# Kernel tuning notes

Measured on AMD Instinct MI355X. Metric: run time of the kernel, lower is better.

Reference implementation:

```python
import jax, jax.numpy as jnp
import numpy as np

DIM = 1024
NUM_HEADS = 16
HEAD_DIM = DIM // NUM_HEADS
BATCH = 4
SEQ = 2048
EPS = 1e-6


def rotate_half(x):
    # interleaved-pair rotation: (..., d) -> view (..., d//2, 2), swap with sign
    x = x.reshape(*x.shape[:-1], -1, 2)
    x1, x2 = jnp.split(x, 2, axis=-1)  # each (..., d//2, 1)
    x = jnp.concatenate([-x2, x1], axis=-1)
    return x.reshape(*x.shape[:-2], -1)


def apply_rope(x, cos, sin):
    # x: [B,S,H,D], cos/sin: [S,D]
    cos = cos[None, :, None, :].astype(x.dtype)
    sin = sin[None, :, None, :].astype(x.dtype)
    return x * cos + rotate_half(x) * sin


def rms_norm(x, w):
    var = jnp.mean(jnp.square(x), axis=-1, keepdims=True)
    return x * jax.lax.rsqrt(var + EPS) * w


def setup_inputs() -> dict:
    key = jax.random.key(0)
    ks = jax.random.split(key, 8)
    s = 0.02
    return {
        "x": jax.random.normal(ks[0], (BATCH, SEQ, DIM), jnp.float32),
        "rope_cos": jnp.cos(jnp.arange(SEQ, dtype=jnp.float32)[:, None] *
                            (1.0 / (10000.0 ** (jnp.repeat(jnp.arange(HEAD_DIM // 2, dtype=jnp.float32), 2) * 2 / HEAD_DIM)))[None, :]),
        "rope_sin": jnp.sin(jnp.arange(SEQ, dtype=jnp.float32)[:, None] *
                            (1.0 / (10000.0 ** (jnp.repeat(jnp.arange(HEAD_DIM // 2, dtype=jnp.float32), 2) * 2 / HEAD_DIM)))[None, :]),
        "qkv_w": jax.random.normal(ks[1], (3 * DIM, DIM), jnp.float32) * s,
        "qkv_b": jax.random.normal(ks[2], (3 * DIM,), jnp.float32) * s,
        "proj_w": jax.random.normal(ks[3], (DIM, DIM), jnp.float32) * s,
        "proj_b": jax.random.normal(ks[4], (DIM,), jnp.float32) * s,
        "q_norm_w": jnp.ones((HEAD_DIM,), jnp.float32),
        "k_norm_w": jnp.ones((HEAD_DIM,), jnp.float32),
    }


def reference(x, rope_cos, rope_sin, qkv_w, qkv_b, proj_w, proj_b, q_norm_w, k_norm_w):
    B, S, C = x.shape
    H, D = NUM_HEADS, HEAD_DIM
    qkv = x @ qkv_w.T + qkv_b                      # [B,S,3C]
    qkv = qkv.reshape(B, S, 3, H, D)
    q, k, v = qkv[:, :, 0], qkv[:, :, 1], qkv[:, :, 2]  # [B,S,H,D]
    q = apply_rope(rms_norm(q, q_norm_w), rope_cos, rope_sin)
    k = apply_rope(rms_norm(k, k_norm_w), rope_cos, rope_sin)
    scale = 1.0 / np.sqrt(D).astype(np.float32)
    attn = jnp.einsum('bqhd,bkhd->bhqk', q.astype(jnp.float32), k.astype(jnp.float32))
    attn = jax.nn.softmax(attn * scale, axis=-1).astype(x.dtype)
    out = jnp.einsum('bhqk,bkhd->bqhd', attn, v).reshape(B, S, C)
    return out @ proj_w.T + proj_b
```

## Files before the change

### kernel.cpp

```cpp
#include <hip/hip_runtime.h>
#include <math.h>
#include <type_traits>

#define DIM 1024
#define NH 16
#define HD 64
#define BATCH 4
#define SEQ 2048
#define EPS 1e-6f

typedef __attribute__((ext_vector_type(8))) short short8;
typedef __attribute__((ext_vector_type(4))) short short4v;
typedef __attribute__((ext_vector_type(4))) float float4v;

__device__ inline unsigned short f2bf(float f) {
    unsigned u = __float_as_uint(f);
    u += 0x7FFF + ((u >> 16) & 1);
    return (unsigned short)(u >> 16);
}
__device__ inline float bf2f(unsigned short b) {
    return __uint_as_float(((unsigned)b) << 16);
}
__device__ inline unsigned pk2bf(float lo, float hi) {
    unsigned ul = __float_as_uint(lo) + 0x8000u;
    unsigned uh = __float_as_uint(hi) + 0x8000u;
    return __builtin_amdgcn_perm(uh, ul, 0x07060302u);
}

#if __has_builtin(__builtin_amdgcn_exp2f)
#define EXP2F(x) __builtin_amdgcn_exp2f(x)
#else
#define EXP2F(x) exp2f(x)
#endif

#if __has_builtin(__builtin_amdgcn_mfma_f32_16x16x16bf16_1k)
__device__ inline float4v mfma16(short4v a, short4v b, float4v c) {
    return __builtin_amdgcn_mfma_f32_16x16x16bf16_1k(a, b, c, 0, 0, 0);
}
#elif __has_builtin(__builtin_amdgcn_mfma_f32_16x16x16_bf16)
__device__ inline float4v mfma16(short4v a, short4v b, float4v c) {
    return __builtin_amdgcn_mfma_f32_16x16x16_bf16(a, b, c, 0, 0, 0);
}
#else
__device__ inline float4v mfma16(short4v a, short4v b, float4v c) {
    asm volatile("v_mfma_f32_16x16x16_bf16 %0, %1, %2, %0\n\ts_nop 4"
                 : "+v"(c) : "v"(a), "v"(b));
    return c;
}
#endif

#define GLDS16(gp, lp) __builtin_amdgcn_global_load_lds( \
    (const __attribute__((address_space(1))) void*)(gp), \
    (__attribute__((address_space(3))) void*)(lp), 16, 0, 0)

__global__ __launch_bounds__(256) void prep_all(
    const float* __restrict__ x, const float* __restrict__ qkv_w,
    const float* __restrict__ proj_w,
    const float* __restrict__ cos_t, const float* __restrict__ sin_t,
    unsigned short* __restrict__ xb, unsigned short* __restrict__ qkvwb,
    unsigned short* __restrict__ projwb, unsigned* __restrict__ csP)
{
    const int bid = blockIdx.x;
    if (bid < 8192) {
        int i = bid * 256 + threadIdx.x;
        float4 f = ((const float4*)x)[i];
        ushort4 o;
        o.x = f2bf(f.x); o.y = f2bf(f.y); o.z = f2bf(f.z); o.w = f2bf(f.w);
        ((ushort4*)xb)[i] = o;
    } else if (bid < 8192 + 3072) {
        const int rn = bid - 8192;
        int ro = rn;
        if (rn < 2048) {
            const int head = rn >> 6, c = rn & 63, j = c >> 4, cl = c & 15;
            ro = (head << 6) + ((j & 1) + 2 * cl + 32 * (j >> 1));
        }
        float4 f = ((const float4*)(qkv_w + (long)ro * DIM))[threadIdx.x];
        ushort4 o;
        o.x = f2bf(f.x); o.y = f2bf(f.y); o.z = f2bf(f.z); o.w = f2bf(f.w);
        ((ushort4*)(qkvwb + (long)rn * DIM))[threadIdx.x] = o;
    } else if (bid < 8192 + 3072 + 1024) {
        int i = (bid - 11264) * 256 + threadIdx.x;
        float4 f = ((const float4*)proj_w)[i];
        ushort4 o;
        o.x = f2bf(f.x); o.y = f2bf(f.y); o.z = f2bf(f.z); o.w = f2bf(f.w);
        ((ushort4*)projwb)[i] = o;
    } else {
        int i = (bid - 12288) * 256 + threadIdx.x;
        int a = i >> 11, s = i & 2047;
        float c = cos_t[s * 64 + 2 * a], sn = sin_t[s * 64 + 2 * a];
        csP[a * SEQ + s] = ((unsigned)f2bf(sn) << 16) | f2bf(c);
    }
}

__global__ __launch_bounds__(256) void gemm_qkv_fused(
    const unsigned short* __restrict__ A, const unsigned short* __restrict__ W,
    const float* __restrict__ bias, const unsigned* __restrict__ csP,
    const float* __restrict__ qw, const float* __restrict__ kw,
    unsigned short* __restrict__ q, unsigned short* __restrict__ k,
    unsigned short* __restrict__ vt)
{
    __shared__ __align__(16) unsigned short As[128 * 32];
    __shared__ __align__(16) unsigned short Bs[128 * 32];

    const int t    = threadIdx.x;
    const int lane = t & 63;
    const int w    = t >> 6;
    const int row0 = blockIdx.y * 128;
    const int col0 = blockIdx.x * 128;
    const int wr   = (w & 1) * 64;
    const int wc   = (w >> 1) * 64;
    const int cl   = lane & 15;
    const int quad = lane >> 4;

    float4v acc[4][4];
#pragma unroll
    for (int i = 0; i < 4; ++i)
#pragma unroll
        for (int j = 0; j < 4; ++j) acc[i][j] = (float4v){0.f, 0.f, 0.f, 0.f};

    const int off1 = t * 16, off2 = 4096 + t * 16;
    const int r1 = off1 >> 6, c1 = off1 & 63;
    const int r2 = off2 >> 6, c2 = off2 & 63;
    const char* Ab = (const char*)A + (long)row0 * DIM * 2;
    const char* Wb = (const char*)W + (long)col0 * DIM * 2;
    const long  ks = DIM * 2;

    for (int k0 = 0; k0 < DIM; k0 += 32) {
        const long kb = (long)k0 * 2;
        GLDS16(Ab + (long)r1 * ks + kb + c1, (char*)As + off1);
        GLDS16(Ab + (long)r2 * ks + kb + c2, (char*)As + off2);
        GLDS16(Wb + (long)r1 * ks + kb + c1, (char*)Bs + off1);
        GLDS16(Wb + (long)r2 * ks + kb + c2, (char*)Bs + off2);
        __syncthreads();

        short8 af[4], bfr[4];
#pragma unroll
        for (int i = 0; i < 4; ++i)
            af[i] = *(const short8*)&As[(wr + i * 16 + cl) * 32 + quad * 8];
#pragma unroll
        for (int j = 0; j < 4; ++j)
            bfr[j] = *(const short8*)&Bs[(wc + j * 16 + cl) * 32 + quad * 8];
#pragma unroll
        for (int i = 0; i < 4; ++i)
#pragma unroll
            for (int j = 0; j < 4; ++j)
                acc[i][j] = __builtin_amdgcn_mfma_f32_16x16x32_bf16(af[i], bfr[j], acc[i][j], 0, 0, 0);
        __syncthreads();
    }

    const int gcol  = col0 + wc;
    const int b     = row0 >> 11;
    const int srow0 = (row0 & 2047) + wr;

    if (gcol < 2 * DIM) {
        const bool isq = (gcol < DIM);
        const int  h   = (isq ? gcol : gcol - DIM) >> 6;
        const float* nw = isq ? qw : kw;
        const float scale = isq ? 0.180336880f : 1.0f;
        unsigned short* dst = (isq ? q : k) + (long)(b * NH + h) * SEQ * 64;

        float bjv[4];
#pragma unroll
        for (int j = 0; j < 4; ++j)
            bjv[j] = bias[gcol + (j & 1) + 2 * cl + 32 * (j >> 1)];
#pragma unroll
        for (int i = 0; i < 4; ++i)
#pragma unroll
            for (int j = 0; j < 4; ++j)
#pragma unroll
                for (int r = 0; r < 4; ++r) acc[i][j][r] += bjv[j];

        float rinv[4][4];
#pragma unroll
        for (int i = 0; i < 4; ++i)
#pragma unroll
            for (int r = 0; r < 4; ++r) {
                float ss = acc[i][0][r] * acc[i][0][r];
                ss = fmaf(acc[i][1][r], acc[i][1][r], ss);
                ss = fmaf(acc[i][2][r], acc[i][2][r], ss);
                ss = fmaf(acc[i][3][r], acc[i][3][r], ss);
                ss += __shfl_xor(ss, 1, 64);
                ss += __shfl_xor(ss, 2, 64);
                ss += __shfl_xor(ss, 4, 64);
                ss += __shfl_xor(ss, 8, 64);
                rinv[i][r] = rsqrtf(ss * (1.f / 64.f) + EPS) * scale;
            }

        const float nwe[2] = { nw[2 * cl],     nw[32 + 2 * cl] };
        const float nwo[2] = { nw[2 * cl + 1], nw[33 + 2 * cl] };

#pragma unroll
        for (int i = 0; i < 4; ++i) {
            const int sb = srow0 + i * 16 + quad * 4;
#pragma unroll
            for (int jp = 0; jp < 2; ++jp) {
                uint4 cs4 = *(const uint4*)(csP + (long)(jp * 16 + cl) * SEQ + sb);
#pragma unroll
                for (int r = 0; r < 4; ++r) {
                    float g  = rinv[i][r];
                    float xe = acc[i][2 * jp][r]     * g * nwe[jp];
                    float xo = acc[i][2 * jp + 1][r] * g * nwo[jp];
                    unsigned u = (r == 0) ? cs4.x : (r == 1) ? cs4.y : (r == 2) ? cs4.z : cs4.w;
                    float c  = bf2f((unsigned short)(u & 0xffff));
                    float sn = bf2f((unsigned short)(u >> 16));
                    float oe = fmaf(xe, c, -(xo * sn));
                    float oo = fmaf(xo, c,   xe * sn);
                    *(unsigned*)(dst + (long)(sb + r) * 64 + jp * 32 + 2 * cl) = pk2bf(oe, oo);
                }
            }
        }
    } else {
        const int h = (gcol - 2 * DIM) >> 6;
        float bjv[4];
#pragma unroll
        for (int j = 0; j < 4; ++j) bjv[j] = bias[gcol + j * 16 + cl];
        unsigned short* vdst = vt + (long)(b * NH + h) * SEQ * 64
                                  + (long)(srow0 >> 6) * 4096;
#pragma unroll
        for (int j = 0; j < 4; ++j)
#pragma unroll
            for (int ip = 0; ip < 2; ++ip) {
                const int i0 = 2 * ip;
                uint4 st;
                st.x = pk2bf(acc[i0][j][0] + bjv[j],     acc[i0][j][1] + bjv[j]);
                st.y = pk2bf(acc[i0][j][2] + bjv[j],     acc[i0][j][3] + bjv[j]);
                st.z = pk2bf(acc[i0 + 1][j][0] + bjv[j], acc[i0 + 1][j][1] + bjv[j]);
                st.w = pk2bf(acc[i0 + 1][j][2] + bjv[j], acc[i0 + 1][j][3] + bjv[j]);
                *(uint4*)(vdst + (j * 2 + ip) * 512 + lane * 8) = st;
            }
    }
}

__global__ __launch_bounds__(256) void gemm_proj(
    const unsigned short* __restrict__ A, const unsigned short* __restrict__ W,
    const float* __restrict__ bias, float* __restrict__ C)
{
    __shared__ __align__(16) unsigned short As[128 * 32];
    __shared__ __align__(16) unsigned short Bs[128 * 32];

    const int t    = threadIdx.x;
    const int lane = t & 63;
    const int w    = t >> 6;
    const int row0 = blockIdx.y * 128;
    const int col0 = blockIdx.x * 128;
    const int wr   = (w & 1) * 64;
    const int wc   = (w >> 1) * 64;

    float4v acc[4][4];
#pragma unroll
    for (int i = 0; i < 4; ++i)
#pragma unroll
        for (int j = 0; j < 4; ++j) acc[i][j] = (float4v){0.f, 0.f, 0.f, 0.f};

    const int off1 = t * 16, off2 = 4096 + t * 16;
    const int r1 = off1 >> 6, c1 = off1 & 63;
    const int r2 = off2 >> 6, c2 = off2 & 63;
    const char* Ab = (const char*)A + (long)row0 * DIM * 2;
    const char* Wb = (const char*)W + (long)col0 * DIM * 2;
    const long  ks = DIM * 2;

    for (int k0 = 0; k0 < DIM; k0 += 32) {
        const long kb = (long)k0 * 2;
        GLDS16(Ab + (long)r1 * ks + kb + c1, (char*)As + off1);
        GLDS16(Ab + (long)r2 * ks + kb + c2, (char*)As + off2);
        GLDS16(Wb + (long)r1 * ks + kb + c1, (char*)Bs + off1);
        GLDS16(Wb + (long)r2 * ks + kb + c2, (char*)Bs + off2);
        __syncthreads();

        short8 af[4], bfr[4];
#pragma unroll
        for (int i = 0; i < 4; ++i)
            af[i] = *(const short8*)&As[(wr + i * 16 + (lane & 15)) * 32 + (lane >> 4) * 8];
#pragma unroll
        for (int j = 0; j < 4; ++j)
            bfr[j] = *(const short8*)&Bs[(wc + j * 16 + (lane & 15)) * 32 + (lane >> 4) * 8];
#pragma unroll
        for (int i = 0; i < 4; ++i)
#pragma unroll
            for (int j = 0; j < 4; ++j)
                acc[i][j] = __builtin_amdgcn_mfma_f32_16x16x32_bf16(af[i], bfr[j], acc[i][j], 0, 0, 0);
        __syncthreads();
    }

    const int qd = lane >> 4, cl = lane & 15;
#pragma unroll
    for (int j = 0; j < 4; ++j) {
        const int col = col0 + wc + j * 16 + cl;
        const float bj = bias[col];
#pragma unroll
        for (int i = 0; i < 4; ++i) {
            const long rr = row0 + wr + i * 16 + qd * 4;
#pragma unroll
            for (int r = 0; r < 4; ++r)
                C[(rr + r) * (long)DIM + col] = acc[i][j][r] + bj;
        }
    }
}

__global__ __launch_bounds__(256) void flash_mfma(
    const unsigned short* __restrict__ q, const unsigned short* __restrict__ k,
    const unsigned short* __restrict__ vt, unsigned short* __restrict__ out)
{
    __shared__ __align__(16) unsigned short Qs[2][128 * 32];
    __shared__ __align__(16) unsigned short Ks[2][64 * 32];
    __shared__ __align__(16) unsigned short Vts[64 * 64];

    const int t    = threadIdx.x;
    const int lane = t & 63;
    const int w    = t >> 6;
    const int bh   = blockIdx.y;
    const int b    = bh >> 4;
    const int h    = bh & 15;
    const int q0   = blockIdx.x * 128;
    const int cl   = lane & 15;
    const int quad = lane >> 4;

    const char* qb  = (const char*)(q  + (long)bh * SEQ * 64);
    const char* kb  = (const char*)(k  + (long)bh * SEQ * 64);
    const char* vtb = (const char*)(vt + (long)bh * SEQ * 64);

#pragma unroll
    for (int rd = 0; rd < 2; ++rd) {
        const int off = rd * 4096 + t * 16;
        const int row = off >> 6, cb = off & 63;
#pragma unroll
        for (int hf = 0; hf < 2; ++hf)
            GLDS16(qb + (long)(q0 + row) * 128 + hf * 64 + cb, (char*)Qs[hf] + off);
    }
    __syncthreads();

    short8 aq[2][2];
#pragma unroll
    for (int qg = 0; qg < 2; ++qg)
#pragma unroll
        for (int hf = 0; hf < 2; ++hf)
            aq[qg][hf] = *(const short8*)&Qs[hf][(w * 32 + qg * 16 + cl) * 32 + quad * 8];

    const short4v ones = (short4v){(short)0x3F80, (short)0x3F80, (short)0x3F80, (short)0x3F80};

    float4v o[2][4], o4[2];
#pragma unroll
    for (int qg = 0; qg < 2; ++qg) {
        o4[qg] = (float4v){0.f, 0.f, 0.f, 0.f};
#pragma unroll
        for (int i = 0; i < 4; ++i) o[qg][i] = (float4v){0.f, 0.f, 0.f, 0.f};
    }

    const int soff = t * 16, srow = soff >> 6, scb = soff & 63;

    for (int kt = 0; kt < SEQ / 64; ++kt) {
#pragma unroll
        for (int hf = 0; hf < 2; ++hf)
            GLDS16(kb + (long)(kt * 64 + srow) * 128 + hf * 64 + scb, (char*)Ks[hf] + soff);
        GLDS16(vtb + (long)kt * 8192 + t * 16,        (char*)Vts + t * 16);
        GLDS16(vtb + (long)kt * 8192 + 4096 + t * 16, (char*)Vts + 4096 + t * 16);
        __syncthreads();

        short4v pa[2][4];
#pragma unroll
        for (int j = 0; j < 4; ++j) {
            short8 a0 = *(const short8*)&Ks[0][(j * 16 + cl) * 32 + quad * 8];
            short8 a1 = *(const short8*)&Ks[1][(j * 16 + cl) * 32 + quad * 8];
#pragma unroll
            for (int qg = 0; qg < 2; ++qg) {
                float4v z = (float4v){0.f, 0.f, 0.f, 0.f};
                z = __builtin_amdgcn_mfma_f32_16x16x32_bf16(a0, aq[qg][0], z, 0, 0, 0);
                float4v s = __builtin_amdgcn_mfma_f32_16x16x32_bf16(a1, aq[qg][1], z, 0, 0, 0);
                float p0 = EXP2F(s[0]), p1 = EXP2F(s[1]);
                float p2 = EXP2F(s[2]), p3 = EXP2F(s[3]);
                unsigned lo = pk2bf(p0, p1), hi = pk2bf(p2, p3);
                pa[qg][j] = __builtin_bit_cast(short4v, ((unsigned long long)hi << 32) | lo);
                o4[qg] = mfma16(ones, pa[qg][j], o4[qg]);
            }
        }

#pragma unroll
        for (int fi = 0; fi < 4; ++fi) {
#pragma unroll
            for (int fjp = 0; fjp < 2; ++fjp) {
                short8 vv = *(const short8*)&Vts[(fi * 2 + fjp) * 512 + lane * 8];
                short4v va = __builtin_shufflevector(vv, vv, 0, 1, 2, 3);
                short4v vb = __builtin_shufflevector(vv, vv, 4, 5, 6, 7);
#pragma unroll
                for (int qg = 0; qg < 2; ++qg) {
                    o[qg][fi] = mfma16(va, pa[qg][2 * fjp],     o[qg][fi]);
                    o[qg][fi] = mfma16(vb, pa[qg][2 * fjp + 1], o[qg][fi]);
                }
            }
        }
        __syncthreads();
    }

#pragma unroll
    for (int qg = 0; qg < 2; ++qg) {
        const float inv = 1.f / o4[qg][0];
        unsigned short* orow = out + ((long)b * SEQ + q0 + w * 32 + qg * 16 + cl) * DIM + h * 64;
#pragma unroll
        for (int i = 0; i < 4; ++i) {
            unsigned lo = pk2bf(o[qg][i][0] * inv, o[qg][i][1] * inv);
            unsigned hi = pk2bf(o[qg][i][2] * inv, o[qg][i][3] * inv);
            ushort4 st = __builtin_bit_cast(ushort4, ((unsigned long long)hi << 32) | lo);
            *(ushort4*)(orow + i * 16 + quad * 4) = st;
        }
    }
}

extern "C" void kernel_launch(void* const* d_in, const int* in_sizes, int n_in,
                              void* d_out, int out_size, void* d_ws, size_t ws_size,
                              hipStream_t stream)
{
    const float* x        = (const float*)d_in[0];
    const float* rope_cos = (const float*)d_in[1];
    const float* rope_sin = (const float*)d_in[2];
    const float* qkv_w    = (const float*)d_in[3];
    const float* qkv_b    = (const float*)d_in[4];
    const float* proj_w   = (const float*)d_in[5];
    const float* proj_b   = (const float*)d_in[6];
    const float* q_norm_w = (const float*)d_in[7];
    const float* k_norm_w = (const float*)d_in[8];
    float* outp = (float*)d_out;

    const int M = BATCH * SEQ;
    char* p = (char*)d_ws;
    unsigned short* xb    = (unsigned short*)p; p += (long)M * DIM * 2;
    unsigned short* qkvwb = (unsigned short*)p; p += (long)3 * DIM * DIM * 2;
    unsigned short* projwb= (unsigned short*)p; p += (long)DIM * DIM * 2;
    unsigned short* qb    = (unsigned short*)p; p += (long)M * DIM * 2;
    unsigned short* kbuf  = (unsigned short*)p; p += (long)M * DIM * 2;
    unsigned short* vtb   = (unsigned short*)p; p += (long)M * DIM * 2;
    unsigned short* attno = (unsigned short*)p; p += (long)M * DIM * 2;
    unsigned*       csP   = (unsigned*)p;       p += (long)32 * SEQ * 4;

    prep_all<<<dim3(12544), 256, 0, stream>>>(
        x, qkv_w, proj_w, rope_cos, rope_sin, xb, qkvwb, projwb, csP);

    gemm_qkv_fused<<<dim3(3 * DIM / 128, M / 128), 256, 0, stream>>>(
        xb, qkvwb, qkv_b, csP, q_norm_w, k_norm_w, qb, kbuf, vtb);

    flash_mfma<<<dim3(SEQ / 128, BATCH * NH), 256, 0, stream>>>(qb, kbuf, vtb, attno);

    gemm_proj<<<dim3(DIM / 128, M / 128), 256, 0, stream>>>(
        attno, projwb, proj_b, outp);
}
```

Before: 302.9 us.

## Load Q/K/V fragments directly from global memory, dropping LDS staging and barriers

```diff
diff --git a/kernel.cpp b/kernel.cpp
--- a/kernel.cpp
+++ b/kernel.cpp
@@ -301,10 +301,6 @@
     const unsigned short* __restrict__ q, const unsigned short* __restrict__ k,
     const unsigned short* __restrict__ vt, unsigned short* __restrict__ out)
 {
-    __shared__ __align__(16) unsigned short Qs[2][128 * 32];
-    __shared__ __align__(16) unsigned short Ks[2][64 * 32];
-    __shared__ __align__(16) unsigned short Vts[64 * 64];
-
     const int t    = threadIdx.x;
     const int lane = t & 63;
     const int w    = t >> 6;
@@ -319,24 +315,16 @@
     const char* kb  = (const char*)(k  + (long)bh * SEQ * 64);
     const char* vtb = (const char*)(vt + (long)bh * SEQ * 64);
 
-#pragma unroll
-    for (int rd = 0; rd < 2; ++rd) {
-        const int off = rd * 4096 + t * 16;
-        const int row = off >> 6, cb = off & 63;
+    short8 aq[2][2];
+#pragma unroll
+    for (int qg = 0; qg < 2; ++qg)
 #pragma unroll
         for (int hf = 0; hf < 2; ++hf)
-            GLDS16(qb + (long)(q0 + row) * 128 + hf * 64 + cb, (char*)Qs[hf] + off);
-    }
-    __syncthreads();
-
-    short8 aq[2][2];
-#pragma unroll
-    for (int qg = 0; qg < 2; ++qg)
-#pragma unroll
-        for (int hf = 0; hf < 2; ++hf)
-            aq[qg][hf] = *(const short8*)&Qs[hf][(w * 32 + qg * 16 + cl) * 32 + quad * 8];
-
-    const short4v ones = (short4v){(short)0x3F80, (short)0x3F80, (short)0x3F80, (short)0x3F80};
+            aq[qg][hf] = *(const short8*)(qb +
+                (long)(q0 + w * 32 + qg * 16 + cl) * 128 + hf * 64 + quad * 16);
+
+    const short4v ones = (short4v){(short)0x3F80, (short)0x3F80,
+                                   (short)0x3F80, (short)0x3F80};
 
     float4v o[2][4], o4[2];
 #pragma unroll
@@ -346,60 +334,68 @@
         for (int i = 0; i < 4; ++i) o[qg][i] = (float4v){0.f, 0.f, 0.f, 0.f};
     }
 
-    const int soff = t * 16, srow = soff >> 6, scb = soff & 63;
-
+#pragma unroll 2
     for (int kt = 0; kt < SEQ / 64; ++kt) {
-#pragma unroll
-        for (int hf = 0; hf < 2; ++hf)
-            GLDS16(kb + (long)(kt * 64 + srow) * 128 + hf * 64 + scb, (char*)Ks[hf] + soff);
-        GLDS16(vtb + (long)kt * 8192 + t * 16,        (char*)Vts + t * 16);
-        GLDS16(vtb + (long)kt * 8192 + 4096 + t * 16, (char*)Vts + 4096 + t * 16);
-        __syncthreads();
-
-        short4v pa[2][4];
-#pragma unroll
-        for (int j = 0; j < 4; ++j) {
-            short8 a0 = *(const short8*)&Ks[0][(j * 16 + cl) * 32 + quad * 8];
-            short8 a1 = *(const short8*)&Ks[1][(j * 16 + cl) * 32 + quad * 8];
+        const char* kbase = kb + (long)kt * 64 * 128;
+        short8 kf[4][2];
+#pragma unroll
+        for (int j = 0; j < 4; ++j)
+#pragma unroll
+            for (int hf = 0; hf < 2; ++hf)
+                kf[j][hf] = *(const short8*)(kbase +
+                    (long)(j * 16 + cl) * 128 + hf * 64 + quad * 16);
+        short8 vf[4][2];
+#pragma unroll
+        for (int fi = 0; fi < 4; ++fi)
+#pragma unroll
+            for (int jp = 0; jp < 2; ++jp)
+                vf[fi][jp] = *(const short8*)(vtb + (long)kt * 8192 +
+                    (fi * 2 + jp) * 1024 + lane * 16);
+
+#pragma unroll
+        for (int jp = 0; jp < 2; ++jp) {
+            short4v pa[2][2];
 #pragma unroll
             for (int qg = 0; qg < 2; ++qg) {
-                float4v z = (float4v){0.f, 0.f, 0.f, 0.f};
-                z = __builtin_amdgcn_mfma_f32_16x16x32_bf16(a0, aq[qg][0], z, 0, 0, 0);
-                float4v s = __builtin_amdgcn_mfma_f32_16x16x32_bf16(a1, aq[qg][1], z, 0, 0, 0);
-                float p0 = EXP2F(s[0]), p1 = EXP2F(s[1]);
-                float p2 = EXP2F(s[2]), p3 = EXP2F(s[3]);
-                unsigned lo = pk2bf(p0, p1), hi = pk2bf(p2, p3);
-                pa[qg][j] = __builtin_bit_cast(short4v, ((unsigned long long)hi << 32) | lo);
-                o4[qg] = mfma16(ones, pa[qg][j], o4[qg]);
+#pragma unroll
+                for (int jj = 0; jj < 2; ++jj) {
+                    const int j = jp * 2 + jj;
+                    float4v z = (float4v){0.f, 0.f, 0.f, 0.f};
+                    z = __builtin_amdgcn_mfma_f32_16x16x32_bf16(kf[j][0], aq[qg][0], z, 0, 0, 0);
+                    z = __builtin_amdgcn_mfma_f32_16x16x32_bf16(kf[j][1], aq[qg][1], z, 0, 0, 0);
+                    float p0 = EXP2F(z[0]), p1 = EXP2F(z[1]);
+                    float p2 = EXP2F(z[2]), p3 = EXP2F(z[3]);
+                    unsigned lo = pk2bf(p0, p1), hi = pk2bf(p2, p3);
+                    pa[qg][jj] = __builtin_bit_cast(short4v,
+                        ((unsigned long long)hi << 32) | lo);
+                    o4[qg] = mfma16(ones, pa[qg][jj], o4[qg]);
+                }
             }
-        }
-
-#pragma unroll
-        for (int fi = 0; fi < 4; ++fi) {
-#pragma unroll
-            for (int fjp = 0; fjp < 2; ++fjp) {
-                short8 vv = *(const short8*)&Vts[(fi * 2 + fjp) * 512 + lane * 8];
+#pragma unroll
+            for (int fi = 0; fi < 4; ++fi) {
+                short8 vv = vf[fi][jp];
                 short4v va = __builtin_shufflevector(vv, vv, 0, 1, 2, 3);
                 short4v vb = __builtin_shufflevector(vv, vv, 4, 5, 6, 7);
 #pragma unroll
                 for (int qg = 0; qg < 2; ++qg) {
-                    o[qg][fi] = mfma16(va, pa[qg][2 * fjp],     o[qg][fi]);
-                    o[qg][fi] = mfma16(vb, pa[qg][2 * fjp + 1], o[qg][fi]);
+                    o[qg][fi] = mfma16(va, pa[qg][0], o[qg][fi]);
+                    o[qg][fi] = mfma16(vb, pa[qg][1], o[qg][fi]);
                 }
             }
         }
-        __syncthreads();
     }
 
 #pragma unroll
     for (int qg = 0; qg < 2; ++qg) {
         const float inv = 1.f / o4[qg][0];
-        unsigned short* orow = out + ((long)b * SEQ + q0 + w * 32 + qg * 16 + cl) * DIM + h * 64;
+        unsigned short* orow = out +
+            ((long)b * SEQ + q0 + w * 32 + qg * 16 + cl) * DIM + h * 64;
 #pragma unroll
         for (int i = 0; i < 4; ++i) {
             unsigned lo = pk2bf(o[qg][i][0] * inv, o[qg][i][1] * inv);
             unsigned hi = pk2bf(o[qg][i][2] * inv, o[qg][i][3] * inv);
-            ushort4 st = __builtin_bit_cast(ushort4, ((unsigned long long)hi << 32) | lo);
+            ushort4 st = __builtin_bit_cast(ushort4,
+                ((unsigned long long)hi << 32) | lo);
             *(ushort4*)(orow + i * 16 + quad * 4) = st;
         }
     }
```

After: 363.5 us. 20.0% more time.
